# Kernel tuning notes

Measured on AMD Instinct MI355X. Metric: run time of the kernel, lower is better.

## Reference

```python
import jax, jax.numpy as jnp
import numpy as np

B, TL, TR, D, L = 32, 256, 256, 256, 32
EPS = 1e-6


def setup_inputs() -> dict:
    key = jax.random.key(0)
    ks = jax.random.split(key, 14)
    f = lambda k, s: jax.random.normal(k, s, dtype=jnp.float32)
    return {
        "lstm_lt": f(ks[0], (B, TL, D)),
        "forward_h_lt": f(ks[1], (B, D // 2)),
        "forward_c_lt": f(ks[2], (B, D // 2)),
        "backward_h_lt": f(ks[3], (B, D // 2)),
        "backward_c_lt": f(ks[4], (B, D // 2)),
        "lstm_rt": f(ks[5], (B, TR, D)),
        "forward_h_rt": f(ks[6], (B, D // 2)),
        "forward_c_rt": f(ks[7], (B, D // 2)),
        "backward_h_rt": f(ks[8], (B, D // 2)),
        "backward_c_rt": f(ks[9], (B, D // 2)),
        "W_full": 0.1 * f(ks[10], (L, D)),
        "W_maxpool": 0.1 * f(ks[11], (L, D)),
        "W_att": 0.1 * f(ks[12], (L, D)),
        "W_maxatt": 0.1 * f(ks[13], (L, D)),
    }


def _cosine_matrix(lt, rt):
    # cosine similarity matrix [B, TL, TR] with eps-clamped norms
    nl = jnp.sqrt(jnp.maximum(jnp.sum(lt * lt, axis=-1), EPS))  # [B, TL]
    nr = jnp.sqrt(jnp.maximum(jnp.sum(rt * rt, axis=-1), EPS))  # [B, TR]
    num = jnp.einsum('bid,bjd->bij', lt, rt)
    return num / nl[:, :, None] / nr[:, None, :]


def reference(lstm_lt, forward_h_lt, forward_c_lt, backward_h_lt, backward_c_lt,
              lstm_rt, forward_h_rt, forward_c_rt, backward_h_rt, backward_c_rt,
              W_full, W_maxpool, W_att, W_maxatt):
    # full matching: tanh(sum_d lt[b,t,d] * W[l,d] * h_rt[b,d]) -> [B, TL, L]
    h_rt = jnp.concatenate([forward_h_rt, backward_h_rt], axis=-1)  # [B, D]
    full = jnp.tanh(jnp.einsum('btd,ld,bd->btl', lstm_lt, W_full, h_rt))

    # max-pooling matching: tanh over [B, TL, TR, L], then max over TR
    mm = jnp.tanh(jnp.einsum('bid,ld,bjd->bijl', lstm_lt, W_maxpool, lstm_rt))
    maxpooling = jnp.max(mm, axis=2)  # [B, TL, L]

    # attentive matching: cosine-weighted sum of rt states (raw sum, as in source)
    scores = _cosine_matrix(lstm_lt, lstm_rt)             # [B, TL, TR]
    att_lt = jnp.einsum('bij,bjd->bid', scores, lstm_rt)  # [B, TL, D]
    attentive = jnp.tanh(jnp.einsum('btd,ld,btd->btl', lstm_lt, W_att, att_lt))
    # max-attentive uses the same attention vector in the source (pooling arg unused)
    max_attentive = jnp.tanh(jnp.einsum('btd,ld,btd->btl', lstm_lt, W_maxatt, att_lt))

    return jnp.concatenate([full, maxpooling, attentive, max_attentive], axis=-1)
```

## Files before the change

kernel.cpp:

```cpp
#include <hip/hip_runtime.h>
#include <hip/hip_bf16.h>
#include <math.h>


typedef __attribute__((ext_vector_type(4)))  float f32x4;
typedef __attribute__((ext_vector_type(16))) float f32x16;
typedef __attribute__((ext_vector_type(8)))  short s16x8;
typedef __attribute__((ext_vector_type(4)))  unsigned short u16x4;
typedef __attribute__((ext_vector_type(8)))  unsigned short u16x8;
typedef unsigned short u16;

#define DEV static __device__ __forceinline__

DEV u16 f2bf(float f) {
  unsigned u = __builtin_bit_cast(unsigned, f);
  return (u16)((u + 0x7FFFu + ((u >> 16) & 1u)) >> 16);
}
DEV float bf2f(u16 s) { return __builtin_bit_cast(float, ((unsigned)s) << 16); }
DEV f32x16 zero16() {
  f32x16 a;
  #pragma unroll
  for (int i = 0; i < 16; ++i) a[i] = 0.f;
  return a;
}

__global__ __launch_bounds__(256) void k_prep_lt(const float* __restrict__ lt,
                                                 float* __restrict__ nl_inv) {
  int w = threadIdx.x >> 6, lane = threadIdx.x & 63;
  int row = blockIdx.x * 4 + w;
  f32x4 v = *(const f32x4*)(lt + (size_t)row * 256 + lane * 4);
  float s = v.x * v.x + v.y * v.y + v.z * v.z + v.w * v.w;
  #pragma unroll
  for (int m = 32; m >= 1; m >>= 1) s += __shfl_xor(s, m);
  if (lane == 0) nl_inv[row] = 1.0f / sqrtf(fmaxf(s, 1e-6f));
}

__global__ __launch_bounds__(256) void k_prep_rt(const float* __restrict__ rt,
                                                 u16* __restrict__ rt_hi,
                                                 u16* __restrict__ rt_lo,
                                                 u16* __restrict__ rtT,
                                                 float* __restrict__ nr_inv) {
  __shared__ u16 ldsT[256][68];
  int b = blockIdx.x >> 2, j0 = (blockIdx.x & 3) * 64;
  int tid = threadIdx.x, w = tid >> 6, lane = tid & 63;
  for (int rep = 0; rep < 16; ++rep) {
    int jl = rep * 4 + w, j = j0 + jl;
    size_t base = ((size_t)b * 256 + j) * 256;
    float ss = 0.f;
    #pragma unroll
    for (int k = 0; k < 4; ++k) {
      int d = lane + k * 64;
      float f = rt[base + d];
      ss += f * f;
      u16 h = f2bf(f);
      rt_hi[base + d] = h;
      rt_lo[base + d] = f2bf(f - bf2f(h));
      ldsT[d][jl] = h;
    }
    #pragma unroll
    for (int m = 32; m >= 1; m >>= 1) ss += __shfl_xor(ss, m);
    if (lane == 0) nr_inv[b * 256 + j] = 1.0f / sqrtf(fmaxf(ss, 1e-6f));
  }
  __syncthreads();
  for (int rep = 0; rep < 16; ++rep) {
    int c = rep * 256 + tid;
    int d = c >> 4, q = c & 15;
    u16x4 v = *(const u16x4*)&ldsT[d][q * 4];
    *(u16x4*)(rtT + ((size_t)b * 256 + d) * 256 + j0 + q * 4) = v;
  }
}

#define ATT_LTH 0
#define ATT_LTL 16384
#define ATT_RTH 32768
#define ATT_RTL 65536
#define ATT_RTT 98304
#define ATT_PH  131072
#define ATT_PL  135168
#define ATT_NLS 139264
#define ATT_NRS 139392
#define ATT_SM  140416

__global__ __launch_bounds__(256) void k_att(const float* __restrict__ lt,
                                             const u16* __restrict__ rt_hi,
                                             const u16* __restrict__ rt_lo,
                                             const u16* __restrict__ rtT,
                                             const float* __restrict__ nl_inv,
                                             const float* __restrict__ nr_inv,
                                             float* __restrict__ att) {
  extern __shared__ char sm[];
  char* LTH = sm + ATT_LTH;  char* LTL = sm + ATT_LTL;
  char* RTH = sm + ATT_RTH;  char* RTL = sm + ATT_RTL;
  char* RTT = sm + ATT_RTT;
  char* PH  = sm + ATT_PH;   char* PL  = sm + ATT_PL;
  float* nls = (float*)(sm + ATT_NLS);
  float* nrs = (float*)(sm + ATT_NRS);

  int b = blockIdx.x >> 3, i0 = (blockIdx.x & 7) * 32;
  int tid = threadIdx.x, w = tid >> 6, lane = tid & 63;

  #pragma unroll
  for (int rep = 0; rep < 8; ++rep) {
    int c = rep * 256 + tid;
    int row = c >> 6, c4 = c & 63;
    f32x4 v = *(const f32x4*)(lt + ((size_t)b * 256 + i0 + row) * 256 + c4 * 4);
    u16x4 h, lo;
    #pragma unroll
    for (int k = 0; k < 4; ++k) { float f = v[k]; h[k] = f2bf(f); lo[k] = f2bf(f - bf2f(h[k])); }
    int off = row * 512 + ((c4 * 8) ^ ((row & 7) << 4));
    *(u16x4*)(LTH + off) = h;
    *(u16x4*)(LTL + off) = lo;
  }
  if (tid < 32) nls[tid] = nl_inv[b * 256 + i0 + tid];
  nrs[tid] = nr_inv[b * 256 + tid];

  int ih = w >> 1;
  f32x4 accv[8];
  #pragma unroll
  for (int i = 0; i < 8; ++i) { accv[i].x = 0; accv[i].y = 0; accv[i].z = 0; accv[i].w = 0; }

  for (int jt = 0; jt < 4; ++jt) {
    int j0 = jt * 64;
    __syncthreads();
    #pragma unroll
    for (int rep = 0; rep < 8; ++rep) {
      int c = rep * 256 + tid;
      int row = c >> 5, s = c & 31;
      size_t g = ((size_t)b * 256 + j0 + row) * 256 + s * 8;
      int off = row * 512 + ((s * 16) ^ ((row & 7) << 4));
      *(u16x8*)(RTH + off) = *(const u16x8*)(rt_hi + g);
      *(u16x8*)(RTL + off) = *(const u16x8*)(rt_lo + g);
    }
    #pragma unroll
    for (int rep = 0; rep < 8; ++rep) {
      int c = rep * 256 + tid;
      int d = c >> 3, s = c & 7;
      *(u16x8*)(RTT + d * 128 + ((s * 16) ^ ((d & 7) << 4))) =
          *(const u16x8*)(rtT + ((size_t)b * 256 + d) * 256 + j0 + s * 8);
    }
    __syncthreads();

    f32x4 S[2];
    #pragma unroll
    for (int t = 0; t < 2; ++t) { S[t].x = 0; S[t].y = 0; S[t].z = 0; S[t].w = 0; }
    int jqs = (w & 1) * 2;
    #pragma unroll
    for (int ks = 0; ks < 8; ++ks) {
      int k2 = (ks * 32 + (lane >> 4) * 8) * 2;
      int ar = ih * 16 + (lane & 15);
      int ab = ar * 512 + (k2 ^ ((ar & 7) << 4));
      s16x8 ah = *(const s16x8*)(LTH + ab);
      s16x8 al = *(const s16x8*)(LTL + ab);
      #pragma unroll
      for (int fj = 0; fj < 2; ++fj) {
        int br = (jqs + fj) * 16 + (lane & 15);
        int bb = br * 512 + (k2 ^ ((br & 7) << 4));
        s16x8 bh = *(const s16x8*)(RTH + bb);
        s16x8 bl = *(const s16x8*)(RTL + bb);
        S[fj] = __builtin_amdgcn_mfma_f32_16x16x32_bf16(ah, bh, S[fj], 0, 0, 0);
        S[fj] = __builtin_amdgcn_mfma_f32_16x16x32_bf16(ah, bl, S[fj], 0, 0, 0);
        S[fj] = __builtin_amdgcn_mfma_f32_16x16x32_bf16(al, bh, S[fj], 0, 0, 0);
      }
    }
    #pragma unroll
    for (int fj = 0; fj < 2; ++fj) {
      #pragma unroll
      for (int r = 0; r < 4; ++r) {
        int i = ih * 16 + (lane >> 4) * 4 + r;
        int j = (jqs + fj) * 16 + (lane & 15);
        float v = S[fj][r] * nls[i] * nrs[j0 + j];
        u16 h = f2bf(v), l2 = f2bf(v - bf2f(h));
        int pb = i * 128 + ((j * 2) ^ ((i & 7) << 4));
        *(u16*)(PH + pb) = h;
        *(u16*)(PL + pb) = l2;
      }
    }
    __syncthreads();

    int db = (w & 1) * 128;
    #pragma unroll
    for (int ks = 0; ks < 2; ++ks) {
      int k2 = (ks * 32 + (lane >> 4) * 8) * 2;
      int pr = ih * 16 + (lane & 15);
      int pb = pr * 128 + (k2 ^ ((pr & 7) << 4));
      s16x8 ph = *(const s16x8*)(PH + pb);
      s16x8 pl = *(const s16x8*)(PL + pb);
      #pragma unroll
      for (int dq = 0; dq < 8; ++dq) {
        int dr = db + dq * 16 + (lane & 15);
        int bb = dr * 128 + (k2 ^ ((dr & 7) << 4));
        s16x8 bv = *(const s16x8*)(RTT + bb);
        accv[dq] = __builtin_amdgcn_mfma_f32_16x16x32_bf16(ph, bv, accv[dq], 0, 0, 0);
        accv[dq] = __builtin_amdgcn_mfma_f32_16x16x32_bf16(pl, bv, accv[dq], 0, 0, 0);
      }
    }
  }
  #pragma unroll
  for (int dq = 0; dq < 8; ++dq) {
    #pragma unroll
    for (int r = 0; r < 4; ++r) {
      int i = i0 + ih * 16 + (lane >> 4) * 4 + r;
      int d = (w & 1) * 128 + dq * 16 + (lane & 15);
      att[((size_t)b * 256 + i) * 256 + d] = accv[dq][r];
    }
  }
}

#define MP_A   0
#define MP_B   65536
#define MP_W   131072
#define MP_RED 132096
#define MP_SM  133120

__global__ __launch_bounds__(256) void k_maxpool(const float* __restrict__ lt,
                                                 const u16* __restrict__ rt_hi,
                                                 const float* __restrict__ Wmp,
                                                 float* __restrict__ out) {
  extern __shared__ char sm[];
  char* A = sm + MP_A;
  char* Bm = sm + MP_B;
  float* wrow = (float*)(sm + MP_W);
  float* red = (float*)(sm + MP_RED);

  int b = blockIdx.x >> 6, rem = blockIdx.x & 63;
  int l = rem >> 1, i0 = (rem & 1) * 128;
  int tid = threadIdx.x, w = tid >> 6, lane = tid & 63;

  wrow[tid] = Wmp[l * 256 + tid];
  __syncthreads();

  #pragma unroll
  for (int rep = 0; rep < 16; ++rep) {
    int c = rep * 256 + tid;
    int row = c >> 5, s = c & 31;
    const float* src = lt + ((size_t)b * 256 + i0 + row) * 256 + s * 8;
    f32x4 v0 = *(const f32x4*)src, v1 = *(const f32x4*)(src + 4);
    f32x4 w0 = *(const f32x4*)(wrow + s * 8), w1 = *(const f32x4*)(wrow + s * 8 + 4);
    u16x8 hv;
    hv[0] = f2bf(v0.x * w0.x); hv[1] = f2bf(v0.y * w0.y);
    hv[2] = f2bf(v0.z * w0.z); hv[3] = f2bf(v0.w * w0.w);
    hv[4] = f2bf(v1.x * w1.x); hv[5] = f2bf(v1.y * w1.y);
    hv[6] = f2bf(v1.z * w1.z); hv[7] = f2bf(v1.w * w1.w);
    *(u16x8*)(A + row * 512 + ((s * 16) ^ ((row & 7) << 4))) = hv;
  }

  int iw = (w >> 1) * 64, jw = (w & 1) * 64;
  float rm[32];
  #pragma unroll
  for (int r = 0; r < 32; ++r) rm[r] = -3.0e38f;

  for (int jt = 0; jt < 2; ++jt) {
    __syncthreads();
    #pragma unroll
    for (int rep = 0; rep < 16; ++rep) {
      int c = rep * 256 + tid;
      int row = c >> 5, s = c & 31;
      *(u16x8*)(Bm + row * 512 + ((s * 16) ^ ((row & 7) << 4))) =
          *(const u16x8*)(rt_hi + ((size_t)b * 256 + jt * 128 + row) * 256 + s * 8);
    }
    __syncthreads();
    f32x16 a00 = zero16(), a01 = zero16(), a10 = zero16(), a11 = zero16();
    #pragma unroll
    for (int ks = 0; ks < 16; ++ks) {
      int k2 = (ks * 16 + (lane >> 5) * 8) * 2;
      int ar0 = iw + (lane & 31), ar1 = ar0 + 32;
      s16x8 fa0 = *(const s16x8*)(A + ar0 * 512 + (k2 ^ ((ar0 & 7) << 4)));
      s16x8 fa1 = *(const s16x8*)(A + ar1 * 512 + (k2 ^ ((ar1 & 7) << 4)));
      int br0 = jw + (lane & 31), br1 = br0 + 32;
      s16x8 fb0 = *(const s16x8*)(Bm + br0 * 512 + (k2 ^ ((br0 & 7) << 4)));
      s16x8 fb1 = *(const s16x8*)(Bm + br1 * 512 + (k2 ^ ((br1 & 7) << 4)));
      a00 = __builtin_amdgcn_mfma_f32_32x32x16_bf16(fa0, fb0, a00, 0, 0, 0);
      a01 = __builtin_amdgcn_mfma_f32_32x32x16_bf16(fa0, fb1, a01, 0, 0, 0);
      a10 = __builtin_amdgcn_mfma_f32_32x32x16_bf16(fa1, fb0, a10, 0, 0, 0);
      a11 = __builtin_amdgcn_mfma_f32_32x32x16_bf16(fa1, fb1, a11, 0, 0, 0);
    }
    #pragma unroll
    for (int r = 0; r < 16; ++r) {
      rm[r]      = fmaxf(rm[r],      fmaxf(a00[r], a01[r]));
      rm[16 + r] = fmaxf(rm[16 + r], fmaxf(a10[r], a11[r]));
    }
  }
  #pragma unroll
  for (int r = 0; r < 32; ++r) {
    float v = rm[r];
    #pragma unroll
    for (int m = 16; m >= 1; m >>= 1) v = fmaxf(v, __shfl_xor(v, m));
    rm[r] = v;
  }
  if ((lane & 31) == 0) {
    int h = lane >> 5;
    #pragma unroll
    for (int fi = 0; fi < 2; ++fi) {
      #pragma unroll
      for (int r = 0; r < 16; ++r) {
        int lrow = iw + fi * 32 + (r & 3) + 8 * (r >> 2) + 4 * h;
        red[(w & 1) * 128 + lrow] = rm[fi * 16 + r];
      }
    }
  }
  __syncthreads();
  if (tid < 128) {
    float m = fmaxf(red[tid], red[128 + tid]);
    out[((size_t)b * 256 + i0 + tid) * 128 + 32 + l] = tanhf(m);
  }
}

#define FN_WF 0
#define FN_WA 33280
#define FN_WM 66560
#define FN_U  99840
#define FN_V  108160
#define FN_HR 116480
#define FN_SM 117504

__global__ __launch_bounds__(256) void k_finals(const float* __restrict__ lt,
                                                const float* __restrict__ fh,
                                                const float* __restrict__ bh,
                                                const float* __restrict__ Wf,
                                                const float* __restrict__ Wa,
                                                const float* __restrict__ Wm,
                                                const float* __restrict__ attw,
                                                float* __restrict__ out) {
  extern __shared__ char sm[];
  float* wf = (float*)(sm + FN_WF);
  float* wa = (float*)(sm + FN_WA);
  float* wm = (float*)(sm + FN_WM);
  float* u  = (float*)(sm + FN_U);
  float* v  = (float*)(sm + FN_V);
  float* hr = (float*)(sm + FN_HR);

  int b = blockIdx.x >> 5, r0 = (blockIdx.x & 31) * 8;
  int tid = threadIdx.x;

  if (tid < 64) {
    int k = tid * 4;
    f32x4 x = (tid < 32) ? *(const f32x4*)(fh + b * 128 + k)
                         : *(const f32x4*)(bh + b * 128 + k - 128);
    *(f32x4*)(hr + k) = x;
  }
  #pragma unroll
  for (int rep = 0; rep < 8; ++rep) {
    int c = rep * 256 + tid;
    int lrow = c >> 6, c4 = c & 63;
    int src = lrow * 256 + c4 * 4, dst = lrow * 260 + c4 * 4;
    *(f32x4*)(wf + dst) = *(const f32x4*)(Wf + src);
    *(f32x4*)(wa + dst) = *(const f32x4*)(Wa + src);
    *(f32x4*)(wm + dst) = *(const f32x4*)(Wm + src);
  }
  __syncthreads();
  #pragma unroll
  for (int rep = 0; rep < 2; ++rep) {
    int c = rep * 256 + tid;
    int row = c >> 6, c4 = c & 63;
    size_t g = ((size_t)b * 256 + r0 + row) * 256 + c4 * 4;
    f32x4 lv = *(const f32x4*)(lt + g);
    f32x4 hv = *(const f32x4*)(hr + c4 * 4);
    f32x4 av = *(const f32x4*)(attw + g);
    *(f32x4*)(u + row * 260 + c4 * 4) = lv * hv;
    *(f32x4*)(v + row * 260 + c4 * 4) = lv * av;
  }
  __syncthreads();
  int r = tid >> 5, l = tid & 31;
  float af = 0.f, aa = 0.f, am = 0.f;
  #pragma unroll 8
  for (int c4 = 0; c4 < 64; ++c4) {
    f32x4 uu = *(const f32x4*)(u + r * 260 + c4 * 4);
    f32x4 vv = *(const f32x4*)(v + r * 260 + c4 * 4);
    f32x4 w1 = *(const f32x4*)(wf + l * 260 + c4 * 4);
    f32x4 w2 = *(const f32x4*)(wa + l * 260 + c4 * 4);
    f32x4 w3 = *(const f32x4*)(wm + l * 260 + c4 * 4);
    af += uu.x * w1.x + uu.y * w1.y + uu.z * w1.z + uu.w * w1.w;
    aa += vv.x * w2.x + vv.y * w2.y + vv.z * w2.z + vv.w * w2.w;
    am += vv.x * w3.x + vv.y * w3.y + vv.z * w3.z + vv.w * w3.w;
  }
  size_t ob = ((size_t)b * 256 + r0 + r) * 128;
  out[ob + l]      = tanhf(af);
  out[ob + 64 + l] = tanhf(aa);
  out[ob + 96 + l] = tanhf(am);
}

extern "C" void kernel_launch(void* const* d_in, const int* in_sizes, int n_in,
                              void* d_out, int out_size, void* d_ws, size_t ws_size,
                              hipStream_t stream) {
  const float* lt  = (const float*)d_in[0];
  const float* rt  = (const float*)d_in[5];
  const float* fh  = (const float*)d_in[6];
  const float* bh  = (const float*)d_in[8];
  const float* Wf  = (const float*)d_in[10];
  const float* Wmp = (const float*)d_in[11];
  const float* Wa  = (const float*)d_in[12];
  const float* Wm  = (const float*)d_in[13];
  float* out = (float*)d_out;

  char* ws = (char*)d_ws;
  u16* rt_hi = (u16*)(ws);
  u16* rt_lo = (u16*)(ws + (4u << 20));
  u16* rtT   = (u16*)(ws + (8u << 20));
  float* att = (float*)(ws + (12u << 20));
  float* nl_inv = (float*)(ws + (20u << 20));
  float* nr_inv = (float*)(ws + (20u << 20) + 32768);

  (void)hipFuncSetAttribute((const void*)k_att,     hipFuncAttributeMaxDynamicSharedMemorySize, ATT_SM);
  (void)hipFuncSetAttribute((const void*)k_maxpool, hipFuncAttributeMaxDynamicSharedMemorySize, MP_SM);
  (void)hipFuncSetAttribute((const void*)k_finals,  hipFuncAttributeMaxDynamicSharedMemorySize, FN_SM);

  k_prep_lt<<<2048, 256, 0, stream>>>(lt, nl_inv);
  k_prep_rt<<<128, 256, 0, stream>>>(rt, rt_hi, rt_lo, rtT, nr_inv);
  k_att<<<256, 256, ATT_SM, stream>>>(lt, rt_hi, rt_lo, rtT, nl_inv, nr_inv, att);
  k_maxpool<<<2048, 256, MP_SM, stream>>>(lt, rt_hi, Wmp, out);
  k_finals<<<1024, 256, FN_SM, stream>>>(lt, fh, bh, Wf, Wa, Wm, att, out);
}
```

Baseline: 236.4 us.

## Keep maxpool A operand in registers and read finals weights from global

The maxpool kernel now builds each wave's W-scaled, bf16-converted lt fragments straight into registers instead of staging them in a 64KB shared-memory tile. This roughly halves its LDS footprint, and launch bounds now request two blocks per CU. Because the row max is reduced and written per j-tile, the running-max registers are gone and the final reduction covers four partial slots. The finals kernel stops copying the three weight matrices into LDS and reads them directly from global/L1, cutting shared memory so more blocks fit. The trade-off is higher VGPR pressure from the 32 register fragments and uncoalesced global weight reads in the dot loop.

```diff
diff --git a/kernel.cpp b/kernel.cpp
--- a/kernel.cpp
+++ b/kernel.cpp
@@ -206,18 +206,16 @@
   }
 }
 
-#define MP_A   0
-#define MP_B   65536
-#define MP_W   131072
-#define MP_RED 132096
-#define MP_SM  133120
-
-__global__ __launch_bounds__(256) void k_maxpool(const float* __restrict__ lt,
-                                                 const u16* __restrict__ rt_hi,
-                                                 const float* __restrict__ Wmp,
-                                                 float* __restrict__ out) {
+#define MP_B   0
+#define MP_W   65536
+#define MP_RED 66560
+#define MP_SM  68608
+
+__global__ __launch_bounds__(256, 2) void k_maxpool(const float* __restrict__ lt,
+                                                    const u16* __restrict__ rt_hi,
+                                                    const float* __restrict__ Wmp,
+                                                    float* __restrict__ out) {
   extern __shared__ char sm[];
-  char* A = sm + MP_A;
   char* Bm = sm + MP_B;
   float* wrow = (float*)(sm + MP_W);
   float* red = (float*)(sm + MP_RED);
@@ -225,29 +223,33 @@
   int b = blockIdx.x >> 6, rem = blockIdx.x & 63;
   int l = rem >> 1, i0 = (rem & 1) * 128;
   int tid = threadIdx.x, w = tid >> 6, lane = tid & 63;
+  int wi = w >> 1, wj = w & 1;
 
   wrow[tid] = Wmp[l * 256 + tid];
   __syncthreads();
 
-  #pragma unroll
-  for (int rep = 0; rep < 16; ++rep) {
-    int c = rep * 256 + tid;
-    int row = c >> 5, s = c & 31;
-    const float* src = lt + ((size_t)b * 256 + i0 + row) * 256 + s * 8;
-    f32x4 v0 = *(const f32x4*)src, v1 = *(const f32x4*)(src + 4);
-    f32x4 w0 = *(const f32x4*)(wrow + s * 8), w1 = *(const f32x4*)(wrow + s * 8 + 4);
-    u16x8 hv;
-    hv[0] = f2bf(v0.x * w0.x); hv[1] = f2bf(v0.y * w0.y);
-    hv[2] = f2bf(v0.z * w0.z); hv[3] = f2bf(v0.w * w0.w);
-    hv[4] = f2bf(v1.x * w1.x); hv[5] = f2bf(v1.y * w1.y);
-    hv[6] = f2bf(v1.z * w1.z); hv[7] = f2bf(v1.w * w1.w);
-    *(u16x8*)(A + row * 512 + ((s * 16) ^ ((row & 7) << 4))) = hv;
-  }
-
-  int iw = (w >> 1) * 64, jw = (w & 1) * 64;
-  float rm[32];
-  #pragma unroll
-  for (int r = 0; r < 32; ++r) rm[r] = -3.0e38f;
+  s16x8 areg[2][16];
+  {
+    int kc0 = (lane >> 5) * 8;
+    #pragma unroll
+    for (int rb = 0; rb < 2; ++rb) {
+      int row = i0 + wi * 64 + rb * 32 + (lane & 31);
+      const float* src = lt + ((size_t)b * 256 + row) * 256 + kc0;
+      #pragma unroll
+      for (int ks = 0; ks < 16; ++ks) {
+        f32x4 v0 = *(const f32x4*)(src + ks * 16);
+        f32x4 v1 = *(const f32x4*)(src + ks * 16 + 4);
+        f32x4 w0 = *(const f32x4*)(wrow + kc0 + ks * 16);
+        f32x4 w1 = *(const f32x4*)(wrow + kc0 + ks * 16 + 4);
+        s16x8 a;
+        a[0] = (short)f2bf(v0.x * w0.x); a[1] = (short)f2bf(v0.y * w0.y);
+        a[2] = (short)f2bf(v0.z * w0.z); a[3] = (short)f2bf(v0.w * w0.w);
+        a[4] = (short)f2bf(v1.x * w1.x); a[5] = (short)f2bf(v1.y * w1.y);
+        a[6] = (short)f2bf(v1.z * w1.z); a[7] = (short)f2bf(v1.w * w1.w);
+        areg[rb][ks] = a;
+      }
+    }
+  }
 
   for (int jt = 0; jt < 2; ++jt) {
     __syncthreads();
@@ -259,59 +261,44 @@
           *(const u16x8*)(rt_hi + ((size_t)b * 256 + jt * 128 + row) * 256 + s * 8);
     }
     __syncthreads();
+
     f32x16 a00 = zero16(), a01 = zero16(), a10 = zero16(), a11 = zero16();
+    int jl0 = wj * 64 + (lane & 31), jl1 = jl0 + 32;
     #pragma unroll
     for (int ks = 0; ks < 16; ++ks) {
       int k2 = (ks * 16 + (lane >> 5) * 8) * 2;
-      int ar0 = iw + (lane & 31), ar1 = ar0 + 32;
-      s16x8 fa0 = *(const s16x8*)(A + ar0 * 512 + (k2 ^ ((ar0 & 7) << 4)));
-      s16x8 fa1 = *(const s16x8*)(A + ar1 * 512 + (k2 ^ ((ar1 & 7) << 4)));
-      int br0 = jw + (lane & 31), br1 = br0 + 32;
-      s16x8 fb0 = *(const s16x8*)(Bm + br0 * 512 + (k2 ^ ((br0 & 7) << 4)));
-      s16x8 fb1 = *(const s16x8*)(Bm + br1 * 512 + (k2 ^ ((br1 & 7) << 4)));
-      a00 = __builtin_amdgcn_mfma_f32_32x32x16_bf16(fa0, fb0, a00, 0, 0, 0);
-      a01 = __builtin_amdgcn_mfma_f32_32x32x16_bf16(fa0, fb1, a01, 0, 0, 0);
-      a10 = __builtin_amdgcn_mfma_f32_32x32x16_bf16(fa1, fb0, a10, 0, 0, 0);
-      a11 = __builtin_amdgcn_mfma_f32_32x32x16_bf16(fa1, fb1, a11, 0, 0, 0);
-    }
-    #pragma unroll
-    for (int r = 0; r < 16; ++r) {
-      rm[r]      = fmaxf(rm[r],      fmaxf(a00[r], a01[r]));
-      rm[16 + r] = fmaxf(rm[16 + r], fmaxf(a10[r], a11[r]));
-    }
-  }
-  #pragma unroll
-  for (int r = 0; r < 32; ++r) {
-    float v = rm[r];
-    #pragma unroll
-    for (int m = 16; m >= 1; m >>= 1) v = fmaxf(v, __shfl_xor(v, m));
-    rm[r] = v;
-  }
-  if ((lane & 31) == 0) {
-    int h = lane >> 5;
-    #pragma unroll
-    for (int fi = 0; fi < 2; ++fi) {
+      s16x8 fb0 = *(const s16x8*)(Bm + jl0 * 512 + (k2 ^ ((jl0 & 7) << 4)));
+      s16x8 fb1 = *(const s16x8*)(Bm + jl1 * 512 + (k2 ^ ((jl1 & 7) << 4)));
+      a00 = __builtin_amdgcn_mfma_f32_32x32x16_bf16(areg[0][ks], fb0, a00, 0, 0, 0);
+      a01 = __builtin_amdgcn_mfma_f32_32x32x16_bf16(areg[0][ks], fb1, a01, 0, 0, 0);
+      a10 = __builtin_amdgcn_mfma_f32_32x32x16_bf16(areg[1][ks], fb0, a10, 0, 0, 0);
+      a11 = __builtin_amdgcn_mfma_f32_32x32x16_bf16(areg[1][ks], fb1, a11, 0, 0, 0);
+    }
+    #pragma unroll
+    for (int rb = 0; rb < 2; ++rb) {
       #pragma unroll
       for (int r = 0; r < 16; ++r) {
-        int lrow = iw + fi * 32 + (r & 3) + 8 * (r >> 2) + 4 * h;
-        red[(w & 1) * 128 + lrow] = rm[fi * 16 + r];
+        float v = (rb == 0) ? fmaxf(a00[r], a01[r]) : fmaxf(a10[r], a11[r]);
+        #pragma unroll
+        for (int m = 16; m >= 1; m >>= 1) v = fmaxf(v, __shfl_xor(v, m));
+        if ((lane & 31) == 0)
+          red[(jt * 2 + wj) * 128 + wi * 64 + rb * 32 +
+              (r & 3) + 8 * (r >> 2) + 4 * (lane >> 5)] = v;
       }
     }
   }
   __syncthreads();
   if (tid < 128) {
-    float m = fmaxf(red[tid], red[128 + tid]);
+    float m = fmaxf(fmaxf(red[tid], red[128 + tid]),
+                    fmaxf(red[256 + tid], red[384 + tid]));
     out[((size_t)b * 256 + i0 + tid) * 128 + 32 + l] = tanhf(m);
   }
 }
 
-#define FN_WF 0
-#define FN_WA 33280
-#define FN_WM 66560
-#define FN_U  99840
-#define FN_V  108160
-#define FN_HR 116480
-#define FN_SM 117504
+#define FN_U  0
+#define FN_V  8320
+#define FN_HR 16640
+#define FN_SM 17664
 
 __global__ __launch_bounds__(256) void k_finals(const float* __restrict__ lt,
                                                 const float* __restrict__ fh,
@@ -322,9 +309,6 @@
                                                 const float* __restrict__ attw,
                                                 float* __restrict__ out) {
   extern __shared__ char sm[];
-  float* wf = (float*)(sm + FN_WF);
-  float* wa = (float*)(sm + FN_WA);
-  float* wm = (float*)(sm + FN_WM);
   float* u  = (float*)(sm + FN_U);
   float* v  = (float*)(sm + FN_V);
   float* hr = (float*)(sm + FN_HR);
@@ -337,15 +321,6 @@
     f32x4 x = (tid < 32) ? *(const f32x4*)(fh + b * 128 + k)
                          : *(const f32x4*)(bh + b * 128 + k - 128);
     *(f32x4*)(hr + k) = x;
-  }
-  #pragma unroll
-  for (int rep = 0; rep < 8; ++rep) {
-    int c = rep * 256 + tid;
-    int lrow = c >> 6, c4 = c & 63;
-    int src = lrow * 256 + c4 * 4, dst = lrow * 260 + c4 * 4;
-    *(f32x4*)(wf + dst) = *(const f32x4*)(Wf + src);
-    *(f32x4*)(wa + dst) = *(const f32x4*)(Wa + src);
-    *(f32x4*)(wm + dst) = *(const f32x4*)(Wm + src);
   }
   __syncthreads();
   #pragma unroll
@@ -366,9 +341,9 @@
   for (int c4 = 0; c4 < 64; ++c4) {
     f32x4 uu = *(const f32x4*)(u + r * 260 + c4 * 4);
     f32x4 vv = *(const f32x4*)(v + r * 260 + c4 * 4);
-    f32x4 w1 = *(const f32x4*)(wf + l * 260 + c4 * 4);
-    f32x4 w2 = *(const f32x4*)(wa + l * 260 + c4 * 4);
-    f32x4 w3 = *(const f32x4*)(wm + l * 260 + c4 * 4);
+    f32x4 w1 = *(const f32x4*)(Wf + l * 256 + c4 * 4);
+    f32x4 w2 = *(const f32x4*)(Wa + l * 256 + c4 * 4);
+    f32x4 w3 = *(const f32x4*)(Wm + l * 256 + c4 * 4);
     af += uu.x * w1.x + uu.y * w1.y + uu.z * w1.z + uu.w * w1.w;
     aa += vv.x * w2.x + vv.y * w2.y + vv.z * w2.z + vv.w * w2.w;
     am += vv.x * w3.x + vv.y * w3.y + vv.z * w3.z + vv.w * w3.w;
```

Result: slower. 402.7 us (+70.3%).
